# Kernel tuning notes

Hardware: AMD Instinct MI355X
Metric: run time of the kernel (lower is better)

## Reference

```python
import jax, jax.numpy as jnp
import numpy as np

H = W = 28
NUM_COUNTS = 10  # iteration counts 0..9, one per logit of determine_n


def conv2d(x, w, b=None, pad=2):
    # x: [B,C,H,W], w: [O,I,5,5]
    y = jax.lax.conv_general_dilated(
        x, w, window_strides=(1, 1), padding=[(pad, pad), (pad, pad)],
        dimension_numbers=("NCHW", "OIHW", "NCHW"))
    if b is not None:
        y = y + b[None, :, None, None]
    return y


def maxpool3(x):
    # kernel 3, stride 3, valid: 28 -> 9
    return jax.lax.reduce_window(
        x, -jnp.inf, jax.lax.max,
        window_dimensions=(1, 1, 3, 3), window_strides=(1, 1, 3, 3),
        padding="VALID")


def setup_inputs() -> dict:
    key = jax.random.key(0)
    ks = jax.random.split(key, 8)
    B = 4096
    s = 0.1
    return {
        "x": jax.random.normal(ks[0], (B, H * W), dtype=jnp.float32),
        "w1": jax.random.normal(ks[1], (8, 1, 5, 5), dtype=jnp.float32) * s,
        "b1": jax.random.normal(ks[2], (8,), dtype=jnp.float32) * s,
        "w2": jax.random.normal(ks[3], (16, 8, 5, 5), dtype=jnp.float32) * s,
        "b2": jax.random.normal(ks[4], (16,), dtype=jnp.float32) * s,
        "fcw": jax.random.normal(ks[5], (10, 16 * 9 * 9), dtype=jnp.float32) * s,
        "fcb": jax.random.normal(ks[6], (10,), dtype=jnp.float32) * s,
        "iterw": jax.random.normal(ks[7], (1, 1, 5, 5), dtype=jnp.float32) * s,
    }


def reference(x, w1, b1, w2, b2, fcw, fcb, iterw):
    B = x.shape[0]
    xi = x.reshape(B, 1, H, W)
    # determine_n: CNN router producing 10 logits over iteration counts
    h = jax.nn.relu(conv2d(xi, w1, b1))
    h = jax.nn.relu(conv2d(h, w2, b2))
    h = maxpool3(h).reshape(B, -1)                      # [B, 1296]
    logits = h @ fcw.T + fcb                            # [B, 10]
    probs = jax.nn.softmax(logits, axis=-1)             # [B, 10]
    # smooth TmIter: expected value over f^n(base), n = 0..9
    def step(y, _):
        return conv2d(y, iterw, None), y
    _, ys = jax.lax.scan(step, xi, None, length=NUM_COUNTS)  # [10,B,1,28,28]
    out = jnp.einsum("bn,nbchw->bchw", probs, ys)
    return out.reshape(B, H, W)
```

## Files before the change

### kernel.cpp

```cpp
#include <hip/hip_runtime.h>
#include <hip/hip_bf16.h>
#include <math.h>
#include <float.h>

typedef __fp16 f16x8  __attribute__((ext_vector_type(8)));
typedef float  f32x16 __attribute__((ext_vector_type(16)));
typedef float  f32x4  __attribute__((ext_vector_type(4)));

#define DY_TAB 0xA524A509A502A540ULL
#define DX_TAB 0x446A444A44924924ULL

__global__ __launch_bounds__(256, 4) void k1_router(
    const float* __restrict__ xg,
    const float* __restrict__ w1g,
    const float* __restrict__ b1g,
    const float* __restrict__ w2g,
    const float* __restrict__ b2g,
    const float* __restrict__ fcwg,
    const float* __restrict__ fcbg,
    float* __restrict__ wsp)
{
    __shared__ __align__(16) char lds[28528];
    float*  spad   = (float*)(lds + 0);
    __fp16* sh1T   = (__fp16*)(lds + 4608);
    __fp16* sw2t   = (__fp16*)(lds + 21968);
    float*  pooled = (float*)(lds + 21968);
    float*  swred  = (float*)(lds + 28368);

    const int tid  = threadIdx.x;
    const int b    = blockIdx.x;
    const int lane = tid & 63;
    const int wid  = tid >> 6;

    f32x4 z4 = {0.f, 0.f, 0.f, 0.f};
    for (int i = tid; i < 92; i += 256) {
        int row, cu;
        if (i < 36) { int r = i / 9; cu = i - 9 * r; row = r < 2 ? r : 28 + r; }
        else        { int j = i - 36; row = 2 + (j >> 1); cu = (j & 1) << 3; }
        ((f32x4*)spad)[row * 9 + cu] = z4;
    }
    for (int i = tid; i < 1085; i += 256) ((f32x4*)sh1T)[i] = z4;
    for (int i = tid; i < 400; i += 256) {
        const int tap = i >> 4, ch = i & 15;
        f16x8 v;
        #pragma unroll
        for (int j = 0; j < 8; ++j) v[j] = (__fp16)w2g[ch * 200 + j * 25 + tap];
        *((f16x8*)(sw2t + i * 8)) = v;
    }
    const int yy = tid / 7, q = tid - yy * 7;
    if (tid < 196) {
        f32x4 v = *((const f32x4*)(xg + (size_t)b * 784 + yy * 28 + q * 4));
        *((f32x4*)(spad + (yy + 2) * 36 + q * 4 + 4)) = v;
    }
    __syncthreads();

    if (tid < 196) {
        float o[8][4];
        #pragma unroll
        for (int c = 0; c < 8; ++c) {
            const float bv = b1g[c];
            #pragma unroll
            for (int px = 0; px < 4; ++px) o[c][px] = bv;
        }
        #pragma unroll
        for (int r = 0; r < 5; ++r) {
            const float* rowp = spad + (yy + r) * 36 + q * 4;
            f32x4 a0 = ((const f32x4*)rowp)[0];
            f32x4 a1 = ((const f32x4*)rowp)[1];
            f32x4 a2 = ((const f32x4*)rowp)[2];
            float u[12] = {a0[0],a0[1],a0[2],a0[3], a1[0],a1[1],a1[2],a1[3],
                           a2[0],a2[1],a2[2],a2[3]};
            #pragma unroll
            for (int c = 0; c < 8; ++c)
                #pragma unroll
                for (int kx = 0; kx < 5; ++kx) {
                    const float w = w1g[c * 25 + r * 5 + kx];
                    #pragma unroll
                    for (int px = 0; px < 4; ++px)
                        o[c][px] = fmaf(u[2 + px + kx], w, o[c][px]);
                }
        }
        #pragma unroll
        for (int px = 0; px < 4; ++px) {
            f16x8 hv;
            #pragma unroll
            for (int c = 0; c < 8; ++c) hv[c] = (__fp16)fmaxf(o[c][px], 0.f);
            *((f16x8*)(sh1T + ((yy + 2) * 35 + (q * 4 + px + 2)) * 8)) = hv;
        }
    }
    const int lr = lane & 31;
    const int g2 = lane >> 5;
    int band = (lr * 57) >> 9; band = band > 2 ? 2 : band;
    const int dy = (int)((DY_TAB >> (2 * lr)) & 3ull);
    const int dx = (int)((DX_TAB >> (2 * lr)) & 3ull);
    const float biasv = (lr < 16) ? b2g[lr] : 0.f;

    f16x8 bfrag[13];
    int   toffB[13];
    #pragma unroll
    for (int s = 0; s < 13; ++s) {
        const int tap = 2 * s + g2;
        const int tapc = tap > 24 ? 24 : tap;
        f16x8 v = *((const f16x8*)(sw2t + (tapc * 16 + (lr & 15)) * 8));
        if (tap > 24 || lr >= 16) {
            #pragma unroll
            for (int j = 0; j < 8; ++j) v[j] = (__fp16)0.f;
        }
        bfrag[s] = v;
        const int ky = (tapc * 13) >> 6;
        const int kx = tapc - 5 * ky;
        toffB[s] = (ky * 35 + kx) * 16;
    }
    __syncthreads();

    for (int tile = wid; tile < 27; tile += 4) {
        const int cell = tile * 3 + band;
        const int cy = (cell * 57) >> 9, cx = cell - 9 * cy;
        const int R0 = 3 * cy + dy, C0 = 3 * cx + dx;
        const char* abase = (const char*)sh1T + (R0 * 35 + C0) * 16;
        f32x16 acc;
        #pragma unroll
        for (int r = 0; r < 16; ++r) acc[r] = biasv;
        #pragma unroll
        for (int s = 0; s < 13; ++s) {
            f16x8 af = *((const f16x8*)(abase + toffB[s]));
            acc = __builtin_amdgcn_mfma_f32_32x32x16_f16(af, bfrag[s], acc, 0, 0, 0);
        }
        float mA, mB, mC;
        if (g2 == 0) {
            mA = fmaxf(fmaxf(fmaxf(acc[0],acc[1]),fmaxf(acc[2],acc[3])), acc[4]);
            mB = fmaxf(fmaxf(fmaxf(acc[5],acc[6]),acc[7]), fmaxf(acc[8],acc[9]));
            mC = fmaxf(fmaxf(fmaxf(acc[10],acc[11]),acc[12]), fmaxf(acc[13],acc[14]));
        } else {
            mA = fmaxf(fmaxf(acc[0],acc[1]),fmaxf(acc[2],acc[3]));
            mB = fmaxf(fmaxf(acc[4],acc[5]),fmaxf(acc[6],acc[7]));
            mC = fmaxf(fmaxf(acc[8],acc[9]),fmaxf(acc[10],acc[11]));
        }
        mA = fmaxf(mA, 0.f); mB = fmaxf(mB, 0.f); mC = fmaxf(mC, 0.f);
        mA = fmaxf(mA, __shfl_xor(mA, 32, 64));
        mB = fmaxf(mB, __shfl_xor(mB, 32, 64));
        mC = fmaxf(mC, __shfl_xor(mC, 32, 64));
        if (g2 == 0 && lr < 16) {
            pooled[lr * 81 + tile * 3 + 0] = mA;
            pooled[lr * 81 + tile * 3 + 1] = mB;
            pooled[lr * 81 + tile * 3 + 2] = mC;
        }
    }
    __syncthreads();

    {
        float part[10];
        #pragma unroll
        for (int j = 0; j < 10; ++j) part[j] = 0.f;
        for (int i4 = tid; i4 < 324; i4 += 256) {
            const f32x4 pv = ((const f32x4*)pooled)[i4];
            #pragma unroll
            for (int j = 0; j < 10; ++j) {
                const f32x4 fw = *((const f32x4*)(fcwg + j * 1296 + i4 * 4));
                part[j] = fmaf(pv[0], fw[0], part[j]);
                part[j] = fmaf(pv[1], fw[1], part[j]);
                part[j] = fmaf(pv[2], fw[2], part[j]);
                part[j] = fmaf(pv[3], fw[3], part[j]);
            }
        }
        #pragma unroll
        for (int j = 0; j < 10; ++j) {
            float v = part[j];
            #pragma unroll
            for (int off = 32; off > 0; off >>= 1) v += __shfl_down(v, off, 64);
            if (lane == 0) swred[wid * 10 + j] = v;
        }
    }
    __syncthreads();

    if (tid == 0) {
        float lg[10]; float mx = -FLT_MAX;
        #pragma unroll
        for (int j = 0; j < 10; ++j) {
            lg[j] = swred[j] + swred[10 + j] + swred[20 + j] + swred[30 + j] + fcbg[j];
            mx = fmaxf(mx, lg[j]);
        }
        float sum = 0.f; float e[10];
        #pragma unroll
        for (int j = 0; j < 10; ++j) { e[j] = expf(lg[j] - mx); sum += e[j]; }
        const float inv = 1.f / sum;
        #pragma unroll
        for (int j = 0; j < 10; ++j) wsp[(size_t)b * 16 + j] = e[j] * inv;
    }
}

__global__ __launch_bounds__(256, 8) void k2_scan(
    const float* __restrict__ xg,
    const float* __restrict__ iwg,
    const float* __restrict__ wsp,
    float* __restrict__ outg)
{
    __shared__ __align__(16) float arena[3456];
    float* spad = arena;
    float* bufA = arena + 1152;
    float* bufB = arena + 2304;

    const int tid = threadIdx.x;
    const int b   = blockIdx.x;

    f32x4 z4 = {0.f, 0.f, 0.f, 0.f};
    for (int i = tid; i < 864; i += 256) ((f32x4*)arena)[i] = z4;
    __syncthreads();

    const int yy = tid / 7, q = tid - yy * 7;
    if (tid < 196) {
        f32x4 v = *((const f32x4*)(xg + (size_t)b * 784 + yy * 28 + q * 4));
        *((f32x4*)(spad + (yy + 2) * 36 + q * 4 + 4)) = v;
    }
    __syncthreads();

    float iw[25];
    #pragma unroll
    for (int k = 0; k < 25; ++k) iw[k] = iwg[k];

    const int rp = tid / 7, qq = tid - rp * 7;
    const float p0 = wsp[(size_t)b * 16];
    float accv[8] = {0.f,0.f,0.f,0.f,0.f,0.f,0.f,0.f};

    const float* cur = spad;
    float* nxt = bufA;
    #pragma unroll 1
    for (int n = 1; n <= 9; ++n) {
        const float pn = wsp[(size_t)b * 16 + n];
        if (tid < 98) {
            float v0[4] = {0.f,0.f,0.f,0.f}, v1[4] = {0.f,0.f,0.f,0.f};
            #pragma unroll
            for (int r = 0; r < 6; ++r) {
                const float* rowp = cur + (2 * rp + r) * 36 + qq * 4;
                f32x4 a0 = ((const f32x4*)rowp)[0];
                f32x4 a1 = ((const f32x4*)rowp)[1];
                f32x4 a2 = ((const f32x4*)rowp)[2];
                float u[12] = {a0[0],a0[1],a0[2],a0[3], a1[0],a1[1],a1[2],a1[3],
                               a2[0],a2[1],a2[2],a2[3]};
                if (n == 1 && r == 2) {
                    #pragma unroll
                    for (int px = 0; px < 4; ++px) accv[px] = p0 * u[4 + px];
                }
                if (n == 1 && r == 3) {
                    #pragma unroll
                    for (int px = 0; px < 4; ++px) accv[4 + px] = p0 * u[4 + px];
                }
                if (r < 5) {
                    #pragma unroll
                    for (int kx = 0; kx < 5; ++kx)
                        #pragma unroll
                        for (int px = 0; px < 4; ++px)
                            v0[px] = fmaf(u[2 + px + kx], iw[r * 5 + kx], v0[px]);
                }
                if (r >= 1) {
                    #pragma unroll
                    for (int kx = 0; kx < 5; ++kx)
                        #pragma unroll
                        for (int px = 0; px < 4; ++px)
                            v1[px] = fmaf(u[2 + px + kx], iw[(r - 1) * 5 + kx], v1[px]);
                }
            }
            if (n < 9) {
                f32x4 w0 = {v0[0], v0[1], v0[2], v0[3]};
                f32x4 w1 = {v1[0], v1[1], v1[2], v1[3]};
                *((f32x4*)(nxt + (2 * rp + 2) * 36 + qq * 4 + 4)) = w0;
                *((f32x4*)(nxt + (2 * rp + 3) * 36 + qq * 4 + 4)) = w1;
            }
            #pragma unroll
            for (int px = 0; px < 4; ++px) {
                accv[px]     = fmaf(pn, v0[px], accv[px]);
                accv[4 + px] = fmaf(pn, v1[px], accv[4 + px]);
            }
        }
        if (n < 9) __syncthreads();
        cur = nxt;
        nxt = (n & 1) ? bufB : bufA;
    }

    if (tid < 98) {
        f32x4 o0 = {accv[0], accv[1], accv[2], accv[3]};
        f32x4 o1 = {accv[4], accv[5], accv[6], accv[7]};
        *((f32x4*)(outg + (size_t)b * 784 + (2 * rp) * 28 + qq * 4))     = o0;
        *((f32x4*)(outg + (size_t)b * 784 + (2 * rp + 1) * 28 + qq * 4)) = o1;
    }
}

extern "C" void kernel_launch(void* const* d_in, const int* in_sizes, int n_in,
                              void* d_out, int out_size, void* d_ws, size_t ws_size,
                              hipStream_t stream) {
    const float* x   = (const float*)d_in[0];
    const float* w1  = (const float*)d_in[1];
    const float* b1  = (const float*)d_in[2];
    const float* w2  = (const float*)d_in[3];
    const float* b2  = (const float*)d_in[4];
    const float* fcw = (const float*)d_in[5];
    const float* fcb = (const float*)d_in[6];
    const float* iw  = (const float*)d_in[7];
    float* out = (float*)d_out;
    float* wsp = (float*)d_ws;
    const int B = in_sizes[0] / 784;
    k1_router<<<B, 256, 0, stream>>>(x, w1, b1, w2, b2, fcw, fcb, wsp);
    k2_scan<<<B, 256, 0, stream>>>(x, iw, wsp, out);
}
```

Before: 114.8 us.

## Interleave two MFMA tiles in router and shrink scan kernel to one wave

In the router kernel, each wave now processes two conv2 tiles at once with two independent accumulator chains. This interleaves MFMA instructions to hide dependency latency, and one leftover tile is handled separately. The scan kernel is reduced from 256 threads to a single 64-thread wave, with each thread computing 4 output rows instead of 2. This reuses loaded rows across more vertical taps and makes the per-iteration barriers cheap, but it raises register use and leaves fewer active lanes per block.

Result: no change. 114.2 us (-0.5%).

```diff
diff --git a/kernel.cpp b/kernel.cpp
--- a/kernel.cpp
+++ b/kernel.cpp
@@ -113,19 +113,12 @@
     }
     __syncthreads();
 
-    for (int tile = wid; tile < 27; tile += 4) {
+    auto tileBase = [&](int tile) -> const char* {
         const int cell = tile * 3 + band;
         const int cy = (cell * 57) >> 9, cx = cell - 9 * cy;
-        const int R0 = 3 * cy + dy, C0 = 3 * cx + dx;
-        const char* abase = (const char*)sh1T + (R0 * 35 + C0) * 16;
-        f32x16 acc;
-        #pragma unroll
-        for (int r = 0; r < 16; ++r) acc[r] = biasv;
-        #pragma unroll
-        for (int s = 0; s < 13; ++s) {
-            f16x8 af = *((const f16x8*)(abase + toffB[s]));
-            acc = __builtin_amdgcn_mfma_f32_32x32x16_f16(af, bfrag[s], acc, 0, 0, 0);
-        }
+        return (const char*)sh1T + ((3 * cy + dy) * 35 + (3 * cx + dx)) * 16;
+    };
+    auto epi = [&](const f32x16& acc, int tile) {
         float mA, mB, mC;
         if (g2 == 0) {
             mA = fmaxf(fmaxf(fmaxf(acc[0],acc[1]),fmaxf(acc[2],acc[3])), acc[4]);
@@ -145,6 +138,36 @@
             pooled[lr * 81 + tile * 3 + 1] = mB;
             pooled[lr * 81 + tile * 3 + 2] = mC;
         }
+    };
+    #pragma unroll 1
+    for (int base = wid; base + 4 < 27; base += 8) {
+        const char* a0 = tileBase(base);
+        const char* a1 = tileBase(base + 4);
+        f32x16 acc0, acc1;
+        #pragma unroll
+        for (int r = 0; r < 16; ++r) { acc0[r] = biasv; acc1[r] = biasv; }
+        #pragma unroll
+        for (int s = 0; s < 13; ++s) {
+            f16x8 af0 = *((const f16x8*)(a0 + toffB[s]));
+            f16x8 af1 = *((const f16x8*)(a1 + toffB[s]));
+            acc0 = __builtin_amdgcn_mfma_f32_32x32x16_f16(af0, bfrag[s], acc0, 0, 0, 0);
+            acc1 = __builtin_amdgcn_mfma_f32_32x32x16_f16(af1, bfrag[s], acc1, 0, 0, 0);
+        }
+        epi(acc0, base);
+        epi(acc1, base + 4);
+    }
+    if (wid < 3) {
+        const int tile = wid + 24;
+        const char* a0 = tileBase(tile);
+        f32x16 acc;
+        #pragma unroll
+        for (int r = 0; r < 16; ++r) acc[r] = biasv;
+        #pragma unroll
+        for (int s = 0; s < 13; ++s) {
+            f16x8 af = *((const f16x8*)(a0 + toffB[s]));
+            acc = __builtin_amdgcn_mfma_f32_32x32x16_f16(af, bfrag[s], acc, 0, 0, 0);
+        }
+        epi(acc, tile);
     }
     __syncthreads();
 
@@ -189,7 +212,7 @@
     }
 }
 
-__global__ __launch_bounds__(256, 8) void k2_scan(
+__global__ __launch_bounds__(64, 4) void k2_scan(
     const float* __restrict__ xg,
     const float* __restrict__ iwg,
     const float* __restrict__ wsp,
@@ -204,11 +227,11 @@
     const int b   = blockIdx.x;
 
     f32x4 z4 = {0.f, 0.f, 0.f, 0.f};
-    for (int i = tid; i < 864; i += 256) ((f32x4*)arena)[i] = z4;
-    __syncthreads();
-
-    const int yy = tid / 7, q = tid - yy * 7;
-    if (tid < 196) {
+    for (int i = tid; i < 864; i += 64) ((f32x4*)arena)[i] = z4;
+    __syncthreads();
+
+    for (int i = tid; i < 196; i += 64) {
+        const int yy = i / 7, q = i - yy * 7;
         f32x4 v = *((const f32x4*)(xg + (size_t)b * 784 + yy * 28 + q * 4));
         *((f32x4*)(spad + (yy + 2) * 36 + q * 4 + 4)) = v;
     }
@@ -220,68 +243,70 @@
 
     const int rp = tid / 7, qq = tid - rp * 7;
     const float p0 = wsp[(size_t)b * 16];
-    float accv[8] = {0.f,0.f,0.f,0.f,0.f,0.f,0.f,0.f};
+    float accv[16];
+    #pragma unroll
+    for (int i = 0; i < 16; ++i) accv[i] = 0.f;
 
     const float* cur = spad;
     float* nxt = bufA;
     #pragma unroll 1
     for (int n = 1; n <= 9; ++n) {
         const float pn = wsp[(size_t)b * 16 + n];
-        if (tid < 98) {
-            float v0[4] = {0.f,0.f,0.f,0.f}, v1[4] = {0.f,0.f,0.f,0.f};
-            #pragma unroll
-            for (int r = 0; r < 6; ++r) {
-                const float* rowp = cur + (2 * rp + r) * 36 + qq * 4;
+        if (tid < 49) {
+            float v[4][4];
+            #pragma unroll
+            for (int rr = 0; rr < 4; ++rr)
+                #pragma unroll
+                for (int px = 0; px < 4; ++px) v[rr][px] = 0.f;
+            #pragma unroll
+            for (int r = 0; r < 8; ++r) {
+                const float* rowp = cur + (4 * rp + r) * 36 + qq * 4;
                 f32x4 a0 = ((const f32x4*)rowp)[0];
                 f32x4 a1 = ((const f32x4*)rowp)[1];
                 f32x4 a2 = ((const f32x4*)rowp)[2];
                 float u[12] = {a0[0],a0[1],a0[2],a0[3], a1[0],a1[1],a1[2],a1[3],
                                a2[0],a2[1],a2[2],a2[3]};
-                if (n == 1 && r == 2) {
+                if (n == 1 && r >= 2 && r <= 5) {
                     #pragma unroll
-                    for (int px = 0; px < 4; ++px) accv[px] = p0 * u[4 + px];
+                    for (int px = 0; px < 4; ++px)
+                        accv[(r - 2) * 4 + px] = p0 * u[4 + px];
                 }
-                if (n == 1 && r == 3) {
-                    #pragma unroll
-                    for (int px = 0; px < 4; ++px) accv[4 + px] = p0 * u[4 + px];
-                }
-                if (r < 5) {
-                    #pragma unroll
-                    for (int kx = 0; kx < 5; ++kx)
+                #pragma unroll
+                for (int rr = 0; rr < 4; ++rr) {
+                    if (rr <= r && r <= rr + 4) {
+                        const int ky = r - rr;
                         #pragma unroll
-                        for (int px = 0; px < 4; ++px)
-                            v0[px] = fmaf(u[2 + px + kx], iw[r * 5 + kx], v0[px]);
-                }
-                if (r >= 1) {
-                    #pragma unroll
-                    for (int kx = 0; kx < 5; ++kx)
-                        #pragma unroll
-                        for (int px = 0; px < 4; ++px)
-                            v1[px] = fmaf(u[2 + px + kx], iw[(r - 1) * 5 + kx], v1[px]);
+                        for (int kx = 0; kx < 5; ++kx)
+                            #pragma unroll
+                            for (int px = 0; px < 4; ++px)
+                                v[rr][px] = fmaf(u[2 + px + kx], iw[ky * 5 + kx], v[rr][px]);
+                    }
                 }
             }
             if (n < 9) {
-                f32x4 w0 = {v0[0], v0[1], v0[2], v0[3]};
-                f32x4 w1 = {v1[0], v1[1], v1[2], v1[3]};
-                *((f32x4*)(nxt + (2 * rp + 2) * 36 + qq * 4 + 4)) = w0;
-                *((f32x4*)(nxt + (2 * rp + 3) * 36 + qq * 4 + 4)) = w1;
+                #pragma unroll
+                for (int rr = 0; rr < 4; ++rr) {
+                    f32x4 w = {v[rr][0], v[rr][1], v[rr][2], v[rr][3]};
+                    *((f32x4*)(nxt + (4 * rp + rr + 2) * 36 + qq * 4 + 4)) = w;
+                }
             }
             #pragma unroll
-            for (int px = 0; px < 4; ++px) {
-                accv[px]     = fmaf(pn, v0[px], accv[px]);
-                accv[4 + px] = fmaf(pn, v1[px], accv[4 + px]);
-            }
+            for (int rr = 0; rr < 4; ++rr)
+                #pragma unroll
+                for (int px = 0; px < 4; ++px)
+                    accv[rr * 4 + px] = fmaf(pn, v[rr][px], accv[rr * 4 + px]);
         }
         if (n < 9) __syncthreads();
         cur = nxt;
         nxt = (n & 1) ? bufB : bufA;
     }
 
-    if (tid < 98) {
-        f32x4 o0 = {accv[0], accv[1], accv[2], accv[3]};
-        f32x4 o1 = {accv[4], accv[5], accv[6], accv[7]};
-        *((f32x4*)(outg + (size_t)b * 784 + (2 * rp) * 28 + qq * 4))     = o0;
-        *((f32x4*)(outg + (size_t)b * 784 + (2 * rp + 1) * 28 + qq * 4)) = o1;
+    if (tid < 49) {
+        #pragma unroll
+        for (int rr = 0; rr < 4; ++rr) {
+            f32x4 o = {accv[rr*4], accv[rr*4+1], accv[rr*4+2], accv[rr*4+3]};
+            *((f32x4*)(outg + (size_t)b * 784 + (4 * rp + rr) * 28 + qq * 4)) = o;
+        }
     }
 }
 
@@ -300,5 +325,5 @@
     float* wsp = (float*)d_ws;
     const int B = in_sizes[0] / 784;
     k1_router<<<B, 256, 0, stream>>>(x, w1, b1, w2, b2, fcw, fcb, wsp);
-    k2_scan<<<B, 256, 0, stream>>>(x, iw, wsp, out);
+    k2_scan<<<B, 64, 0, stream>>>(x, iw, wsp, out);
 }
```
